# Optimization experiments

Measured on AMD Instinct MI355X. Metric: run time of the kernel, lower is better.

Reference implementation:

```python
import jax, jax.numpy as jnp
import numpy as np

N, E = 50000, 1600000
IN_DIM, HID, L, H = 300, 256, 3, 4
HD = HID // H  # 64
EPS = 1e-5


def setup_inputs() -> dict:
    key = jax.random.key(0)
    ks = jax.random.split(key, 24)
    s = 0.02
    inp = {
        'node_feats': jax.random.normal(ks[0], (N, IN_DIM), jnp.float32),
        'role': jax.random.randint(ks[1], (N,), 0, 3),
        'edge_src': jax.random.randint(ks[2], (E,), 0, N),
        'edge_dst': jax.random.randint(ks[3], (E,), 0, N),
        'edge_weights': jax.random.uniform(ks[4], (E,), jnp.float32),
        # input role transforms (question / entity / context)
        'Wq': jax.random.normal(ks[5], (IN_DIM, HID), jnp.float32) * s,
        'bq': jnp.zeros((HID,), jnp.float32),
        'We': jax.random.normal(ks[6], (IN_DIM, HID), jnp.float32) * s,
        'be': jnp.zeros((HID,), jnp.float32),
        'Wc': jax.random.normal(ks[7], (IN_DIM, HID), jnp.float32) * s,
        'bc': jnp.zeros((HID,), jnp.float32),
        # per-head value projections [H, HID, HD] (q/k projections omitted:
        # softmax over a scalar == 1.0, so they never affect output or grads)
        'Wv': jax.random.normal(ks[8], (H, HID, HD), jnp.float32) * s,
        'bv': jnp.zeros((H, HD), jnp.float32),
        # shared 'default' edge-type transform (the torch code always falls
        # through to 'default' because edata['rel'] entries are tensors)
        'Wd': jax.random.normal(ks[9], (HD, HD), jnp.float32) * s,
        'bd': jnp.zeros((HD,), jnp.float32),
        # attention_output
        'Wo': jax.random.normal(ks[10], (HID, HID), jnp.float32) * s,
        'bo': jnp.zeros((HID,), jnp.float32),
        # GRUCell params (torch layout: [3*HID, in], gate order r,z,n)
        'W_ih': jax.random.normal(ks[11], (3 * HID, HID), jnp.float32) * s,
        'W_hh': jax.random.normal(ks[12], (3 * HID, HID), jnp.float32) * s,
        'b_ih': jnp.zeros((3 * HID,), jnp.float32),
        'b_hh': jnp.zeros((3 * HID,), jnp.float32),
        # per-layer LayerNorm affine params [L, HID]
        'ln_w': jnp.ones((L, HID), jnp.float32),
        'ln_b': jnp.zeros((L, HID), jnp.float32),
    }
    return inp


def _layernorm(x, w, b):
    mu = jnp.mean(x, -1, keepdims=True)
    var = jnp.mean(jnp.square(x - mu), -1, keepdims=True)
    return (x - mu) * jax.lax.rsqrt(var + EPS) * w + b


def _gru_cell(x, hprev, W_ih, W_hh, b_ih, b_hh):
    gi = x @ W_ih.T + b_ih
    gh = hprev @ W_hh.T + b_hh
    i_r, i_z, i_n = jnp.split(gi, 3, axis=-1)
    h_r, h_z, h_n = jnp.split(gh, 3, axis=-1)
    r = jax.nn.sigmoid(i_r + h_r)
    z = jax.nn.sigmoid(i_z + h_z)
    n = jnp.tanh(i_n + r * h_n)
    return (1.0 - z) * n + z * hprev


def reference(node_feats, role, edge_src, edge_dst, edge_weights,
              Wq, bq, We, be, Wc, bc, Wv, bv, Wd, bd, Wo, bo,
              W_ih, W_hh, b_ih, b_hh, ln_w, ln_b):
    n_nodes = node_feats.shape[0]
    # role-dependent input transform: 0=question, 1=evidence/answer, 2=other
    hq = node_feats @ Wq + bq
    he = node_feats @ We + be
    hc = node_feats @ Wc + bc
    r = role[:, None]
    h = jax.nn.relu(jnp.where(r == 0, hq, jnp.where(r == 1, he, hc)))

    path_mem = jax.lax.stop_gradient(h)  # .detach().clone()
    prev_h = h
    num_layers, num_heads = ln_w.shape[0], Wv.shape[0]
    for layer in range(num_layers):
        head_msgs = []
        for hd in range(num_heads):
            # value proj + shared 'default' edge transform (node-level, fused)
            vt = (h @ Wv[hd] + bv[hd]) @ Wd + bd  # [N, HD]
            # scalar softmax == 1.0 -> attn_weight == edge_weight
            msg = vt[edge_src] * edge_weights[:, None]  # [E, HD]
            head_msgs.append(jax.ops.segment_sum(msg, edge_dst,
                                                 num_segments=n_nodes))
        combined = jnp.concatenate(head_msgs, axis=-1)  # [N, HID]
        path_mem = _gru_cell(combined, path_mem, W_ih, W_hh, b_ih, b_hh)
        h = _layernorm(prev_h + combined @ Wo + bo, ln_w[layer], ln_b[layer])
        # dropout: identity in eval mode
        prev_h = h
    return h + path_mem
```

## Files before the change

### kernel.cpp

```cpp
#include <hip/hip_runtime.h>
#include <math.h>

#define NN 50000
#define EE 1600000
#define IND 300
#define KPAD 320
#define NL 3
#define NBLK 785

typedef unsigned short u16;
typedef __attribute__((ext_vector_type(8))) short short8;
typedef __attribute__((ext_vector_type(4))) float floatx4;

__device__ __forceinline__ float b2f(u16 u) {
  union { unsigned i; float f; } v; v.i = ((unsigned)u) << 16; return v.f;
}
__device__ __forceinline__ u16 f2b(float f) {
  union { unsigned i; float f; } v; v.f = f;
  unsigned b = v.i; b += 0x7fffu + ((b >> 16) & 1u);
  return (u16)(b >> 16);
}
__device__ __forceinline__ float sigf(float x) { return 1.0f / (1.0f + __expf(-x)); }

__global__ void count_kernel(const int* __restrict__ dst, int* __restrict__ cnt) {
  int e = blockIdx.x * 256 + threadIdx.x;
  if (e < EE) atomicAdd(&cnt[dst[e]], 1);
}

__global__ __launch_bounds__(256) void scan1_kernel(const int* __restrict__ cnt,
                                                    int* __restrict__ rs,
                                                    int* __restrict__ bsum) {
  __shared__ int ws[4];
  const int t = threadIdx.x, l = t & 63, w = t >> 6;
  const int base = blockIdx.x * 2048 + t * 8;
  int v[8];
  int tot = 0;
  #pragma unroll
  for (int k = 0; k < 8; ++k) {
    int i = base + k;
    v[k] = (i < NN) ? cnt[i] : 0;
    tot += v[k];
  }
  int x = tot;
  #pragma unroll
  for (int off = 1; off < 64; off <<= 1) {
    int y = __shfl_up(x, off);
    if (l >= off) x += y;
  }
  if (l == 63) ws[w] = x;
  __syncthreads();
  int wpre = 0;
  for (int q = 0; q < w; ++q) wpre += ws[q];
  int run = wpre + (x - tot);
  #pragma unroll
  for (int k = 0; k < 8; ++k) {
    int i = base + k;
    if (i < NN) rs[i] = run;
    run += v[k];
  }
  if (t == 255) bsum[blockIdx.x] = wpre + x;
}

__global__ void scan2_kernel(int* __restrict__ bsum, int nb) {
  int l = threadIdx.x;
  int v = (l < nb) ? bsum[l] : 0;
  int x = v;
  #pragma unroll
  for (int off = 1; off < 64; off <<= 1) {
    int y = __shfl_up(x, off);
    if (l >= off) x += y;
  }
  if (l < nb) bsum[l] = x - v;
  if (l == 63) bsum[nb] = x;
}

__global__ void scan3_kernel(const int* __restrict__ bsum, int* __restrict__ rs, int nb) {
  int i = blockIdx.x * 256 + threadIdx.x;
  if (i < NN) rs[i] += bsum[i >> 11];
  if (i == 0) rs[NN] = bsum[nb];
}

__global__ void fill_kernel(const int* __restrict__ dst, const int* __restrict__ rs,
                            int* __restrict__ ncnt, const int* __restrict__ esrc,
                            const float* __restrict__ ew, int2* __restrict__ srcw) {
  int e = blockIdx.x * 256 + threadIdx.x;
  if (e < EE) {
    int d = dst[e];
    int p = atomicAdd(&ncnt[d], 1);
    int2 v;
    v.x = esrc[e];
    v.y = __float_as_int(ew[e]);
    srcw[rs[d] + p] = v;
  }
}

__global__ void role_count(const int* __restrict__ role, int* __restrict__ cnt3) {
  __shared__ int lc[3];
  if (threadIdx.x < 3) lc[threadIdx.x] = 0;
  __syncthreads();
  int i = blockIdx.x * 256 + threadIdx.x;
  if (i < NN) atomicAdd(&lc[role[i]], 1);
  __syncthreads();
  if (threadIdx.x < 3) atomicAdd(&cnt3[threadIdx.x], lc[threadIdx.x]);
}

__global__ void role_plan(const int* __restrict__ cnt3, int* __restrict__ pbase,
                          int* __restrict__ blkrole) {
  __shared__ int pb[4];
  if (threadIdx.x == 0) {
    pb[0] = 0;
    for (int b = 0; b < 3; ++b) pb[b + 1] = pb[b] + (((cnt3[b] + 63) >> 6) << 6);
    for (int b = 0; b < 4; ++b) pbase[b] = pb[b];
  }
  __syncthreads();
  for (int blk = threadIdx.x; blk < NBLK; blk += 256) {
    int m0 = blk * 64;
    int r = -1;
    for (int b = 0; b < 3; ++b)
      if (m0 >= pb[b] && m0 < pb[b + 1]) r = b;
    blkrole[blk] = r;
  }
}

__global__ void role_fill(const int* __restrict__ role, const int* __restrict__ pbase,
                          int* __restrict__ pos3, int* __restrict__ perm) {
  __shared__ int lcnt[3], lbase[3];
  int i = blockIdx.x * 256 + threadIdx.x;
  if (threadIdx.x < 3) lcnt[threadIdx.x] = 0;
  __syncthreads();
  int r = 0, lr = 0;
  bool valid = (i < NN);
  if (valid) {
    r = role[i];
    lr = atomicAdd(&lcnt[r], 1);
  }
  __syncthreads();
  if (threadIdx.x < 3) lbase[threadIdx.x] = atomicAdd(&pos3[threadIdx.x], lcnt[threadIdx.x]);
  __syncthreads();
  if (valid) perm[pbase[r] + lbase[r] + lr] = i;
}

__global__ void xcast_kernel(const float* __restrict__ X, u16* __restrict__ Xb) {
  size_t i = (size_t)blockIdx.x * 256 + threadIdx.x;
  if (i >= (size_t)NN * KPAD) return;
  int r = (int)(i / KPAD), k = (int)(i % KPAD);
  Xb[i] = (k < IND) ? f2b(X[(size_t)r * IND + k]) : (u16)0;
}

__global__ void wt3_kernel(const float* __restrict__ Wq, const float* __restrict__ We,
                           const float* __restrict__ Wc, u16* __restrict__ Wqt,
                           u16* __restrict__ Wet, u16* __restrict__ Wct) {
  int n = blockIdx.x;
  int which = blockIdx.y;
  const float* W = (which == 0) ? Wq : (which == 1) ? We : Wc;
  u16* Wt = (which == 0) ? Wqt : (which == 1) ? Wet : Wct;
  for (int k = threadIdx.x; k < KPAD; k += 256)
    Wt[(size_t)n * KPAD + k] = (k < IND) ? f2b(W[(size_t)k * 256 + n]) : (u16)0;
}

__global__ void wallt_kernel(const float* __restrict__ Wv, const float* __restrict__ Wd,
                             u16* __restrict__ Wallt) {
  int i = blockIdx.x;
  int c = threadIdx.x;
  int hd = c >> 6, j = c & 63;
  const float* wv = &Wv[hd * (256 * 64) + i * 64];
  float s = 0.f;
  #pragma unroll
  for (int m = 0; m < 64; ++m) s = fmaf(wv[m], Wd[m * 64 + j], s);
  Wallt[(size_t)c * 256 + i] = f2b(s);
}

__global__ void ball_kernel(const float* __restrict__ bv, const float* __restrict__ Wd,
                            const float* __restrict__ bd, float* __restrict__ ball) {
  int c = threadIdx.x;
  int hd = c >> 6, j = c & 63;
  float s = bd[j];
  #pragma unroll
  for (int m = 0; m < 64; ++m) s = fmaf(bv[hd * 64 + m], Wd[m * 64 + j], s);
  ball[c] = s;
}

__global__ void wot_kernel(const float* __restrict__ Wo, u16* __restrict__ Wot) {
  int n = blockIdx.x;
  int k = threadIdx.x;
  Wot[(size_t)n * 256 + k] = f2b(Wo[(size_t)k * 256 + n]);
}

__global__ void castbf2_kernel(const float* __restrict__ s0, const float* __restrict__ s1,
                               u16* __restrict__ d0, u16* __restrict__ d1) {
  int i = blockIdx.x * 256 + threadIdx.x;
  const int n = 768 * 256;
  if (i < n) d0[i] = f2b(s0[i]);
  else if (i < 2 * n) d1[i - n] = f2b(s1[i - n]);
}

#define GEMM_PROLOG \
  __shared__ __align__(16) u16 As[64][72]; \
  __shared__ __align__(16) u16 Bs[64][72]; \
  const int t = threadIdx.x; \
  const int lane = t & 63; \
  const int wv_ = t >> 6; \
  const int wr = wv_ >> 1, wc = wv_ & 1; \
  const int l15 = lane & 15, l4 = lane >> 4; \
  const int srow = t >> 2; \
  const int scol = (t & 3) << 4;

#define STAGE_A(AG, ASTRIDE, VALID, ROWIDX, K0) { \
  int4 v0 = {0, 0, 0, 0}, v1 = {0, 0, 0, 0}; \
  if (VALID) { \
    const int4* p_ = (const int4*)&(AG)[(size_t)(ROWIDX) * (ASTRIDE) + (K0) + scol]; \
    v0 = p_[0]; v1 = p_[1]; \
  } \
  *(int4*)&As[srow][scol] = v0; \
  *(int4*)&As[srow][scol + 8] = v1; }

#define STAGE_B(BG, BSTRIDE, ROWIDX, K0) { \
  const int4* p_ = (const int4*)&(BG)[(size_t)(ROWIDX) * (BSTRIDE) + (K0) + scol]; \
  *(int4*)&Bs[srow][scol] = p_[0]; \
  *(int4*)&Bs[srow][scol + 8] = p_[1]; }

#define MFMA_STEP(ACC) { \
  _Pragma("unroll") \
  for (int kc = 0; kc < 2; ++kc) { \
    short8 a0_ = *(const short8*)&As[wr * 32 + 0 + l15][kc * 32 + l4 * 8]; \
    short8 a1_ = *(const short8*)&As[wr * 32 + 16 + l15][kc * 32 + l4 * 8]; \
    short8 b0_ = *(const short8*)&Bs[wc * 32 + 0 + l15][kc * 32 + l4 * 8]; \
    short8 b1_ = *(const short8*)&Bs[wc * 32 + 16 + l15][kc * 32 + l4 * 8]; \
    ACC[0][0] = __builtin_amdgcn_mfma_f32_16x16x32_bf16(a0_, b0_, ACC[0][0], 0, 0, 0); \
    ACC[0][1] = __builtin_amdgcn_mfma_f32_16x16x32_bf16(a0_, b1_, ACC[0][1], 0, 0, 0); \
    ACC[1][0] = __builtin_amdgcn_mfma_f32_16x16x32_bf16(a1_, b0_, ACC[1][0], 0, 0, 0); \
    ACC[1][1] = __builtin_amdgcn_mfma_f32_16x16x32_bf16(a1_, b1_, ACC[1][1], 0, 0, 0); \
  } }

#define GEMM128_PROLOG \
  __shared__ __align__(16) u16 As[128][72]; \
  __shared__ __align__(16) u16 Bs[128][72]; \
  const int t = threadIdx.x; \
  const int lane = t & 63; \
  const int wv_ = t >> 6; \
  const int qr = (wv_ >> 1) * 64, qc = (wv_ & 1) * 64; \
  const int l15 = lane & 15, l4 = lane >> 4; \
  const int srow = t >> 1; \
  const int scol = (t & 1) * 32;

#define STAGE128_A(AG, ASTRIDE, VALID, ROWIDX, K0) { \
  int4 v0 = {0,0,0,0}, v1 = {0,0,0,0}, v2 = {0,0,0,0}, v3 = {0,0,0,0}; \
  if (VALID) { \
    const int4* p_ = (const int4*)&(AG)[(size_t)(ROWIDX) * (ASTRIDE) + (K0) + scol]; \
    v0 = p_[0]; v1 = p_[1]; v2 = p_[2]; v3 = p_[3]; \
  } \
  *(int4*)&As[srow][scol] = v0; *(int4*)&As[srow][scol + 8] = v1; \
  *(int4*)&As[srow][scol + 16] = v2; *(int4*)&As[srow][scol + 24] = v3; }

#define STAGE128_B(BG, BSTRIDE, ROWIDX, K0) { \
  const int4* p_ = (const int4*)&(BG)[(size_t)(ROWIDX) * (BSTRIDE) + (K0) + scol]; \
  *(int4*)&Bs[srow][scol] = p_[0]; *(int4*)&Bs[srow][scol + 8] = p_[1]; \
  *(int4*)&Bs[srow][scol + 16] = p_[2]; *(int4*)&Bs[srow][scol + 24] = p_[3]; }

#define MFMA128_STEP(ACC) { \
  _Pragma("unroll") \
  for (int kc = 0; kc < 2; ++kc) { \
    short8 af_[4], bf_[4]; \
    _Pragma("unroll") \
    for (int m = 0; m < 4; ++m) af_[m] = *(const short8*)&As[qr + m * 16 + l15][kc * 32 + l4 * 8]; \
    _Pragma("unroll") \
    for (int n = 0; n < 4; ++n) bf_[n] = *(const short8*)&Bs[qc + n * 16 + l15][kc * 32 + l4 * 8]; \
    _Pragma("unroll") \
    for (int m = 0; m < 4; ++m) \
      _Pragma("unroll") \
      for (int n = 0; n < 4; ++n) \
        ACC[m][n] = __builtin_amdgcn_mfma_f32_16x16x32_bf16(af_[m], bf_[n], ACC[m][n], 0, 0, 0); \
  } }

__global__ __launch_bounds__(256) void proj_mfma(
    const u16* __restrict__ Xb, const int* __restrict__ perm,
    const int* __restrict__ blkrole,
    const u16* __restrict__ Wqt, const u16* __restrict__ Wet, const u16* __restrict__ Wct,
    const float* __restrict__ bq, const float* __restrict__ be, const float* __restrict__ bc,
    u16* __restrict__ h, u16* __restrict__ pm) {
  const int brole = blkrole[blockIdx.y];
  if (brole < 0) return;
  GEMM_PROLOG
  const int m0 = blockIdx.y * 64;
  const int n0 = blockIdx.x * 64;
  const u16* Bt = (brole == 0) ? Wqt : (brole == 1) ? Wet : Wct;
  const float* bb = (brole == 0) ? bq : (brole == 1) ? be : bc;
  const int prow = perm[m0 + srow];
  floatx4 acc[2][2] = {};
  for (int k0 = 0; k0 < KPAD; k0 += 64) {
    STAGE_A(Xb, KPAD, prow >= 0, prow, k0)
    STAGE_B(Bt, KPAD, n0 + srow, k0)
    __syncthreads();
    MFMA_STEP(acc)
    __syncthreads();
  }
  #pragma unroll
  for (int m = 0; m < 2; ++m)
    #pragma unroll
    for (int reg = 0; reg < 4; ++reg) {
      int gr = m0 + wr * 32 + m * 16 + l4 * 4 + reg;
      int pr = perm[gr];
      if (pr >= 0) {
        #pragma unroll
        for (int n = 0; n < 2; ++n) {
          int c = n0 + wc * 32 + n * 16 + l15;
          float vo = fmaxf(acc[m][n][reg] + bb[c], 0.f);
          u16 ub = f2b(vo);
          h[(size_t)pr * 256 + c] = ub;
          pm[(size_t)pr * 256 + c] = ub;
        }
      }
    }
}

__global__ __launch_bounds__(256) void vgemm_mfma(
    const u16* __restrict__ A, const u16* __restrict__ Bt,
    const float* __restrict__ bias, u16* __restrict__ C) {
  GEMM128_PROLOG
  const int m0 = blockIdx.y * 128;
  const int n0 = blockIdx.x * 128;
  const int ar = m0 + srow;
  floatx4 acc[4][4] = {};
  for (int k0 = 0; k0 < 256; k0 += 64) {
    STAGE128_A(A, 256, ar < NN, ar, k0)
    STAGE128_B(Bt, 256, n0 + srow, k0)
    __syncthreads();
    MFMA128_STEP(acc)
    __syncthreads();
  }
  #pragma unroll
  for (int m = 0; m < 4; ++m)
    #pragma unroll
    for (int reg = 0; reg < 4; ++reg) {
      int gr = m0 + qr + m * 16 + l4 * 4 + reg;
      if (gr < NN) {
        #pragma unroll
        for (int n = 0; n < 4; ++n) {
          int c = n0 + qc + n * 16 + l15;
          C[(size_t)gr * 256 + c] = f2b(acc[m][n][reg] + bias[c]);
        }
      }
    }
}

__global__ __launch_bounds__(256) void agg_kernel(
    const int2* __restrict__ srcw, const int* __restrict__ rs,
    const u16* __restrict__ V, u16* __restrict__ comb) {
  int n = blockIdx.x * 4 + (threadIdx.x >> 6);
  int l = threadIdx.x & 63;
  if (n >= NN) return;
  int s = rs[n], e = rs[n + 1];
  float a0 = 0.f, a1 = 0.f, a2 = 0.f, a3 = 0.f;
  float c0 = 0.f, c1 = 0.f, c2 = 0.f, c3 = 0.f;
  const size_t loff = (size_t)l * 4;
  for (int base = s; base < e; base += 64) {
    int2 p = {0, 0};
    if (base + l < e) p = srcw[base + l];
    int cnt = min(64, e - base);
    int j = 0;
    for (; j + 4 <= cnt; j += 4) {
      int s0 = __shfl(p.x, j + 0), s1 = __shfl(p.x, j + 1);
      int s2 = __shfl(p.x, j + 2), s3 = __shfl(p.x, j + 3);
      float w0 = __int_as_float(__shfl(p.y, j + 0));
      float w1 = __int_as_float(__shfl(p.y, j + 1));
      float w2 = __int_as_float(__shfl(p.y, j + 2));
      float w3 = __int_as_float(__shfl(p.y, j + 3));
      ushort4 v0 = *(const ushort4*)&V[(size_t)s0 * 256 + loff];
      ushort4 v1 = *(const ushort4*)&V[(size_t)s1 * 256 + loff];
      ushort4 v2 = *(const ushort4*)&V[(size_t)s2 * 256 + loff];
      ushort4 v3 = *(const ushort4*)&V[(size_t)s3 * 256 + loff];
      a0 = fmaf(w0, b2f(v0.x), a0); a1 = fmaf(w0, b2f(v0.y), a1);
      a2 = fmaf(w0, b2f(v0.z), a2); a3 = fmaf(w0, b2f(v0.w), a3);
      c0 = fmaf(w1, b2f(v1.x), c0); c1 = fmaf(w1, b2f(v1.y), c1);
      c2 = fmaf(w1, b2f(v1.z), c2); c3 = fmaf(w1, b2f(v1.w), c3);
      a0 = fmaf(w2, b2f(v2.x), a0); a1 = fmaf(w2, b2f(v2.y), a1);
      a2 = fmaf(w2, b2f(v2.z), a2); a3 = fmaf(w2, b2f(v2.w), a3);
      c0 = fmaf(w3, b2f(v3.x), c0); c1 = fmaf(w3, b2f(v3.y), c1);
      c2 = fmaf(w3, b2f(v3.z), c2); c3 = fmaf(w3, b2f(v3.w), c3);
    }
    for (; j < cnt; ++j) {
      int src = __shfl(p.x, j);
      float w = __int_as_float(__shfl(p.y, j));
      ushort4 v = *(const ushort4*)&V[(size_t)src * 256 + loff];
      a0 = fmaf(w, b2f(v.x), a0); a1 = fmaf(w, b2f(v.y), a1);
      a2 = fmaf(w, b2f(v.z), a2); a3 = fmaf(w, b2f(v.w), a3);
    }
  }
  a0 += c0; a1 += c1; a2 += c2; a3 += c3;
  ushort4 o;
  o.x = f2b(a0); o.y = f2b(a1); o.z = f2b(a2); o.w = f2b(a3);
  *(ushort4*)&comb[(size_t)n * 256 + loff] = o;
}

__global__ __launch_bounds__(256) void grurz_mfma(
    const u16* __restrict__ comb, const u16* __restrict__ pmc,
    const u16* __restrict__ Wiht, const u16* __restrict__ Whht,
    const float* __restrict__ bih, const float* __restrict__ bhh,
    u16* __restrict__ R, u16* __restrict__ Z) {
  GEMM128_PROLOG
  const int m0 = blockIdx.y * 128;
  const int j0 = blockIdx.x * 128;
  const int ar = m0 + srow;
  floatx4 acc[4][4] = {};
  #pragma unroll
  for (int p = 0; p < 2; ++p) {
    const u16* Ag = p ? pmc : comb;
    const u16* Bt = p ? Whht : Wiht;
    for (int k0 = 0; k0 < 256; k0 += 64) {
      STAGE128_A(Ag, 256, ar < NN, ar, k0)
      STAGE128_B(Bt, 256, j0 + srow, k0)
      __syncthreads();
      MFMA128_STEP(acc)
      __syncthreads();
    }
  }
  #pragma unroll
  for (int m = 0; m < 4; ++m)
    #pragma unroll
    for (int reg = 0; reg < 4; ++reg) {
      int gr = m0 + qr + m * 16 + l4 * 4 + reg;
      if (gr < NN) {
        #pragma unroll
        for (int n = 0; n < 4; ++n) {
          int j = j0 + qc + n * 16 + l15;
          float g = sigf(acc[m][n][reg] + bih[j] + bhh[j]);
          if (j < 256) R[(size_t)gr * 256 + j] = f2b(g);
          else         Z[(size_t)gr * 256 + (j - 256)] = f2b(g);
        }
      }
    }
}

__global__ __launch_bounds__(256) void grun_mfma(
    const u16* __restrict__ comb, const u16* __restrict__ pmc,
    const u16* __restrict__ Wiht, const u16* __restrict__ Whht,
    const float* __restrict__ bih, const float* __restrict__ bhh,
    const u16* __restrict__ R, const u16* __restrict__ Z,
    u16* __restrict__ pmn) {
  GEMM128_PROLOG
  const int m0 = blockIdx.y * 128;
  const int n0 = blockIdx.x * 128;
  const int ar = m0 + srow;
  floatx4 ai[4][4] = {};
  floatx4 ah[4][4] = {};
  for (int k0 = 0; k0 < 256; k0 += 64) {
    STAGE128_A(comb, 256, ar < NN, ar, k0)
    STAGE128_B(Wiht, 256, 512 + n0 + srow, k0)
    __syncthreads();
    MFMA128_STEP(ai)
    __syncthreads();
  }
  for (int k0 = 0; k0 < 256; k0 += 64) {
    STAGE128_A(pmc, 256, ar < NN, ar, k0)
    STAGE128_B(Whht, 256, 512 + n0 + srow, k0)
    __syncthreads();
    MFMA128_STEP(ah)
    __syncthreads();
  }
  #pragma unroll
  for (int m = 0; m < 4; ++m)
    #pragma unroll
    for (int reg = 0; reg < 4; ++reg) {
      int gr = m0 + qr + m * 16 + l4 * 4 + reg;
      if (gr < NN) {
        #pragma unroll
        for (int n = 0; n < 4; ++n) {
          int c = n0 + qc + n * 16 + l15;
          float i_n = ai[m][n][reg] + bih[512 + c];
          float h_n = ah[m][n][reg] + bhh[512 + c];
          float rg = b2f(R[(size_t)gr * 256 + c]);
          float z = b2f(Z[(size_t)gr * 256 + c]);
          float po = b2f(pmc[(size_t)gr * 256 + c]);
          float nn2 = tanhf(i_n + rg * h_n);
          pmn[(size_t)gr * 256 + c] = f2b((1.f - z) * nn2 + z * po);
        }
      }
    }
}

__global__ __launch_bounds__(256) void wo_mfma(
    const u16* __restrict__ comb, const u16* __restrict__ Wot,
    const float* __restrict__ bo, const u16* __restrict__ h,
    u16* __restrict__ tmp) {
  GEMM128_PROLOG
  const int m0 = blockIdx.y * 128;
  const int n0 = blockIdx.x * 128;
  const int ar = m0 + srow;
  floatx4 acc[4][4] = {};
  for (int k0 = 0; k0 < 256; k0 += 64) {
    STAGE128_A(comb, 256, ar < NN, ar, k0)
    STAGE128_B(Wot, 256, n0 + srow, k0)
    __syncthreads();
    MFMA128_STEP(acc)
    __syncthreads();
  }
  #pragma unroll
  for (int m = 0; m < 4; ++m)
    #pragma unroll
    for (int reg = 0; reg < 4; ++reg) {
      int gr = m0 + qr + m * 16 + l4 * 4 + reg;
      if (gr < NN) {
        #pragma unroll
        for (int n = 0; n < 4; ++n) {
          int c = n0 + qc + n * 16 + l15;
          float v = acc[m][n][reg] + bo[c] + b2f(h[(size_t)gr * 256 + c]);
          tmp[(size_t)gr * 256 + c] = f2b(v);
        }
      }
    }
}

__global__ __launch_bounds__(256) void ln_kernel(
    const u16* __restrict__ tmp, u16* __restrict__ h,
    const float* __restrict__ lnw, const float* __restrict__ lnb) {
  int n = blockIdx.x * 4 + (threadIdx.x >> 6);
  int l = threadIdx.x & 63;
  if (n >= NN) return;
  ushort4 v = *(const ushort4*)&tmp[(size_t)n * 256 + l * 4];
  float x0 = b2f(v.x), x1 = b2f(v.y), x2 = b2f(v.z), x3 = b2f(v.w);
  float s = x0 + x1 + x2 + x3;
  #pragma unroll
  for (int off = 1; off < 64; off <<= 1) s += __shfl_xor(s, off);
  float mu = s * (1.f / 256.f);
  float d0 = x0 - mu, d1 = x1 - mu, d2 = x2 - mu, d3 = x3 - mu;
  float vs = d0 * d0 + d1 * d1 + d2 * d2 + d3 * d3;
  #pragma unroll
  for (int off = 1; off < 64; off <<= 1) vs += __shfl_xor(vs, off);
  float inv = rsqrtf(vs * (1.f / 256.f) + 1e-5f);
  int c = l * 4;
  ushort4 o;
  o.x = f2b(d0 * inv * lnw[c + 0] + lnb[c + 0]);
  o.y = f2b(d1 * inv * lnw[c + 1] + lnb[c + 1]);
  o.z = f2b(d2 * inv * lnw[c + 2] + lnb[c + 2]);
  o.w = f2b(d3 * inv * lnw[c + 3] + lnb[c + 3]);
  *(ushort4*)&h[(size_t)n * 256 + c] = o;
}

__global__ __launch_bounds__(256) void ln_final_kernel(
    const u16* __restrict__ tmp, const u16* __restrict__ pm,
    const float* __restrict__ lnw, const float* __restrict__ lnb,
    float* __restrict__ out) {
  int n = blockIdx.x * 4 + (threadIdx.x >> 6);
  int l = threadIdx.x & 63;
  if (n >= NN) return;
  ushort4 v = *(const ushort4*)&tmp[(size_t)n * 256 + l * 4];
  float x0 = b2f(v.x), x1 = b2f(v.y), x2 = b2f(v.z), x3 = b2f(v.w);
  float s = x0 + x1 + x2 + x3;
  #pragma unroll
  for (int off = 1; off < 64; off <<= 1) s += __shfl_xor(s, off);
  float mu = s * (1.f / 256.f);
  float d0 = x0 - mu, d1 = x1 - mu, d2 = x2 - mu, d3 = x3 - mu;
  float vs = d0 * d0 + d1 * d1 + d2 * d2 + d3 * d3;
  #pragma unroll
  for (int off = 1; off < 64; off <<= 1) vs += __shfl_xor(vs, off);
  float inv = rsqrtf(vs * (1.f / 256.f) + 1e-5f);
  int c = l * 4;
  ushort4 pv = *(const ushort4*)&pm[(size_t)n * 256 + c];
  float4 o;
  o.x = b2f(f2b(d0 * inv * lnw[c + 0] + lnb[c + 0])) + b2f(pv.x);
  o.y = b2f(f2b(d1 * inv * lnw[c + 1] + lnb[c + 1])) + b2f(pv.y);
  o.z = b2f(f2b(d2 * inv * lnw[c + 2] + lnb[c + 2])) + b2f(pv.z);
  o.w = b2f(f2b(d3 * inv * lnw[c + 3] + lnb[c + 3])) + b2f(pv.w);
  *(float4*)&out[(size_t)n * 256 + c] = o;
}

extern "C" void kernel_launch(void* const* d_in, const int* in_sizes, int n_in,
                              void* d_out, int out_size, void* d_ws, size_t ws_size,
                              hipStream_t stream) {
  const float* node_feats = (const float*)d_in[0];
  const int* role = (const int*)d_in[1];
  const int* esrc = (const int*)d_in[2];
  const int* edst = (const int*)d_in[3];
  const float* ew = (const float*)d_in[4];
  const float* Wq = (const float*)d_in[5];
  const float* bq = (const float*)d_in[6];
  const float* We = (const float*)d_in[7];
  const float* be = (const float*)d_in[8];
  const float* Wc = (const float*)d_in[9];
  const float* bc = (const float*)d_in[10];
  const float* Wv = (const float*)d_in[11];
  const float* bv = (const float*)d_in[12];
  const float* Wd = (const float*)d_in[13];
  const float* bd = (const float*)d_in[14];
  const float* Wo = (const float*)d_in[15];
  const float* bo = (const float*)d_in[16];
  const float* Wih = (const float*)d_in[17];
  const float* Whh = (const float*)d_in[18];
  const float* bih = (const float*)d_in[19];
  const float* bhh = (const float*)d_in[20];
  const float* lnw = (const float*)d_in[21];
  const float* lnb = (const float*)d_in[22];
  float* out = (float*)d_out;

  char* ws = (char*)d_ws;
  size_t off = 0;
  auto take = [&](size_t bytes) {
    char* p = ws + off;
    off = (off + bytes + 511) & ~(size_t)511;
    return p;
  };
  const size_t NC2 = (size_t)NN * 256 * 2;
  u16* Xb = (u16*)take((size_t)NN * KPAD * 2);
  u16* h = (u16*)take(NC2);
  u16* pm0 = (u16*)take(NC2);
  u16* pm1 = (u16*)take(NC2);
  u16* V = (u16*)take(NC2);
  u16* comb = (u16*)take(NC2);
  u16* Z = (u16*)take(NC2);
  u16* tmp = (u16*)take(NC2);
  u16* Wqt = (u16*)take((size_t)256 * KPAD * 2);
  u16* Wet = (u16*)take((size_t)256 * KPAD * 2);
  u16* Wct = (u16*)take((size_t)256 * KPAD * 2);
  u16* Wallt = (u16*)take((size_t)256 * 256 * 2);
  u16* Wot = (u16*)take((size_t)256 * 256 * 2);
  u16* Wiht = (u16*)take((size_t)768 * 256 * 2);
  u16* Whht = (u16*)take((size_t)768 * 256 * 2);
  float* ball = (float*)take(256 * 4);
  int* cnt = (int*)take((size_t)NN * 4);
  int* rs = (int*)take((size_t)(NN + 1) * 4);
  int* ncnt = (int*)take((size_t)NN * 4);
  int2* srcw = (int2*)take((size_t)EE * 8);
  int* cnt3 = (int*)take(16);
  int* pos3 = (int*)take(16);
  int* pbase = (int*)take(16);
  int* blkrole = (int*)take((size_t)NBLK * 4);
  int* perm = (int*)take((size_t)NBLK * 64 * 4);
  int* bsum = (int*)take(64 * 4);
  u16* R = V;

  const int NB_SCAN = (NN + 2047) / 2048;

  hipMemsetAsync(cnt, 0, (size_t)NN * 4, stream);
  hipMemsetAsync(ncnt, 0, (size_t)NN * 4, stream);
  hipMemsetAsync(cnt3, 0, 16, stream);
  hipMemsetAsync(pos3, 0, 16, stream);
  hipMemsetAsync(perm, 0xFF, (size_t)NBLK * 64 * 4, stream);

  count_kernel<<<(EE + 255) / 256, 256, 0, stream>>>(edst, cnt);
  scan1_kernel<<<NB_SCAN, 256, 0, stream>>>(cnt, rs, bsum);
  scan2_kernel<<<1, 64, 0, stream>>>(bsum, NB_SCAN);
  scan3_kernel<<<(NN + 255) / 256, 256, 0, stream>>>(bsum, rs, NB_SCAN);
  fill_kernel<<<(EE + 255) / 256, 256, 0, stream>>>(edst, rs, ncnt, esrc, ew, srcw);

  role_count<<<(NN + 255) / 256, 256, 0, stream>>>(role, cnt3);
  role_plan<<<1, 256, 0, stream>>>(cnt3, pbase, blkrole);
  role_fill<<<(NN + 255) / 256, 256, 0, stream>>>(role, pbase, pos3, perm);

  xcast_kernel<<<(int)(((size_t)NN * KPAD + 255) / 256), 256, 0, stream>>>(node_feats, Xb);
  wt3_kernel<<<dim3(256, 3), 256, 0, stream>>>(Wq, We, Wc, Wqt, Wet, Wct);
  wallt_kernel<<<256, 256, 0, stream>>>(Wv, Wd, Wallt);
  ball_kernel<<<1, 256, 0, stream>>>(bv, Wd, bd, ball);
  wot_kernel<<<256, 256, 0, stream>>>(Wo, Wot);
  castbf2_kernel<<<(2 * 768 * 256 + 255) / 256, 256, 0, stream>>>(Wih, Whh, Wiht, Whht);

  proj_mfma<<<dim3(4, NBLK), 256, 0, stream>>>(Xb, perm, blkrole, Wqt, Wet, Wct,
                                               bq, be, bc, h, pm0);

  u16* pmc = pm0;
  u16* pmn = pm1;
  const int MB128 = (NN + 127) / 128;
  for (int layer = 0; layer < NL; ++layer) {
    vgemm_mfma<<<dim3(2, MB128), 256, 0, stream>>>(h, Wallt, ball, V);
    agg_kernel<<<(NN + 3) / 4, 256, 0, stream>>>(srcw, rs, V, comb);
    grurz_mfma<<<dim3(4, MB128), 256, 0, stream>>>(comb, pmc, Wiht, Whht, bih, bhh, R, Z);
    grun_mfma<<<dim3(2, MB128), 256, 0, stream>>>(comb, pmc, Wiht, Whht, bih, bhh, R, Z, pmn);
    wo_mfma<<<dim3(2, MB128), 256, 0, stream>>>(comb, Wot, bo, h, tmp);
    if (layer < NL - 1) {
      ln_kernel<<<(NN + 3) / 4, 256, 0, stream>>>(tmp, h, lnw + layer * 256, lnb + layer * 256);
    } else {
      ln_final_kernel<<<(NN + 3) / 4, 256, 0, stream>>>(tmp, pmn, lnw + layer * 256,
                                                        lnb + layer * 256, out);
    }
    u16* sw = pmc; pmc = pmn; pmn = sw;
  }
}
```

Baseline: 1.190 ms.

## Fuse GRU gate kernels into one MFMA kernel and split aggregation by column half

Merges the two GRU kernels (r/z gates, then n gate) into a single MFMA kernel. Each block computes all six gate tiles for 64 rows by 64 columns, so the R and Z intermediate bf16 buffers are never written to or read back from global memory. It also splits the edge aggregation into two column-half launches. Each wave now loads 2 bf16 values per edge instead of 4, which doubles the number of blocks and the edge-index re-reads but gives finer gathers. The fused GEMM uses smaller 64-row tiles with larger LDS use and more accumulators, which may reduce occupancy.

```diff
diff --git a/kernel.cpp b/kernel.cpp
--- a/kernel.cpp
+++ b/kernel.cpp
@@ -7,6 +7,7 @@
 #define KPAD 320
 #define NL 3
 #define NBLK 785
+#define AGG_NB 12500
 
 typedef unsigned short u16;
 typedef __attribute__((ext_vector_type(8))) short short8;
@@ -346,13 +347,15 @@
 __global__ __launch_bounds__(256) void agg_kernel(
     const int2* __restrict__ srcw, const int* __restrict__ rs,
     const u16* __restrict__ V, u16* __restrict__ comb) {
-  int n = blockIdx.x * 4 + (threadIdx.x >> 6);
+  int bid = blockIdx.x;
+  int slice = (bid >= AGG_NB) ? 1 : 0;
+  int nb = bid - slice * AGG_NB;
+  int n = nb * 4 + (threadIdx.x >> 6);
   int l = threadIdx.x & 63;
   if (n >= NN) return;
   int s = rs[n], e = rs[n + 1];
-  float a0 = 0.f, a1 = 0.f, a2 = 0.f, a3 = 0.f;
-  float c0 = 0.f, c1 = 0.f, c2 = 0.f, c3 = 0.f;
-  const size_t loff = (size_t)l * 4;
+  const size_t coff = (size_t)(slice << 7) + l * 2;
+  float a0 = 0.f, a1 = 0.f, c0 = 0.f, c1 = 0.f;
   for (int base = s; base < e; base += 64) {
     int2 p = {0, 0};
     if (base + l < e) p = srcw[base + l];
@@ -365,113 +368,114 @@
       float w1 = __int_as_float(__shfl(p.y, j + 1));
       float w2 = __int_as_float(__shfl(p.y, j + 2));
       float w3 = __int_as_float(__shfl(p.y, j + 3));
-      ushort4 v0 = *(const ushort4*)&V[(size_t)s0 * 256 + loff];
-      ushort4 v1 = *(const ushort4*)&V[(size_t)s1 * 256 + loff];
-      ushort4 v2 = *(const ushort4*)&V[(size_t)s2 * 256 + loff];
-      ushort4 v3 = *(const ushort4*)&V[(size_t)s3 * 256 + loff];
+      ushort2 v0 = *(const ushort2*)&V[(size_t)s0 * 256 + coff];
+      ushort2 v1 = *(const ushort2*)&V[(size_t)s1 * 256 + coff];
+      ushort2 v2 = *(const ushort2*)&V[(size_t)s2 * 256 + coff];
+      ushort2 v3 = *(const ushort2*)&V[(size_t)s3 * 256 + coff];
       a0 = fmaf(w0, b2f(v0.x), a0); a1 = fmaf(w0, b2f(v0.y), a1);
-      a2 = fmaf(w0, b2f(v0.z), a2); a3 = fmaf(w0, b2f(v0.w), a3);
       c0 = fmaf(w1, b2f(v1.x), c0); c1 = fmaf(w1, b2f(v1.y), c1);
-      c2 = fmaf(w1, b2f(v1.z), c2); c3 = fmaf(w1, b2f(v1.w), c3);
       a0 = fmaf(w2, b2f(v2.x), a0); a1 = fmaf(w2, b2f(v2.y), a1);
-      a2 = fmaf(w2, b2f(v2.z), a2); a3 = fmaf(w2, b2f(v2.w), a3);
       c0 = fmaf(w3, b2f(v3.x), c0); c1 = fmaf(w3, b2f(v3.y), c1);
-      c2 = fmaf(w3, b2f(v3.z), c2); c3 = fmaf(w3, b2f(v3.w), c3);
     }
     for (; j < cnt; ++j) {
       int src = __shfl(p.x, j);
       float w = __int_as_float(__shfl(p.y, j));
-      ushort4 v = *(const ushort4*)&V[(size_t)src * 256 + loff];
+      ushort2 v = *(const ushort2*)&V[(size_t)src * 256 + coff];
       a0 = fmaf(w, b2f(v.x), a0); a1 = fmaf(w, b2f(v.y), a1);
-      a2 = fmaf(w, b2f(v.z), a2); a3 = fmaf(w, b2f(v.w), a3);
-    }
-  }
-  a0 += c0; a1 += c1; a2 += c2; a3 += c3;
-  ushort4 o;
-  o.x = f2b(a0); o.y = f2b(a1); o.z = f2b(a2); o.w = f2b(a3);
-  *(ushort4*)&comb[(size_t)n * 256 + loff] = o;
-}
-
-__global__ __launch_bounds__(256) void grurz_mfma(
+    }
+  }
+  a0 += c0; a1 += c1;
+  ushort2 o;
+  o.x = f2b(a0); o.y = f2b(a1);
+  *(ushort2*)&comb[(size_t)n * 256 + coff] = o;
+}
+
+__global__ __launch_bounds__(256) void gru_mfma(
     const u16* __restrict__ comb, const u16* __restrict__ pmc,
     const u16* __restrict__ Wiht, const u16* __restrict__ Whht,
     const float* __restrict__ bih, const float* __restrict__ bhh,
-    u16* __restrict__ R, u16* __restrict__ Z) {
-  GEMM128_PROLOG
-  const int m0 = blockIdx.y * 128;
-  const int j0 = blockIdx.x * 128;
+    u16* __restrict__ pmn) {
+  __shared__ __align__(16) u16 As[2][64][72];
+  __shared__ __align__(16) u16 Bs[6][64][72];
+  const int t = threadIdx.x;
+  const int lane = t & 63;
+  const int wv_ = t >> 6;
+  const int wr = wv_ >> 1, wc = wv_ & 1;
+  const int l15 = lane & 15, l4 = lane >> 4;
+  const int srow = t >> 2;
+  const int scol = (t & 3) << 4;
+  const int m0 = blockIdx.y * 64;
+  const int cb = blockIdx.x;
   const int ar = m0 + srow;
-  floatx4 acc[4][4] = {};
-  #pragma unroll
-  for (int p = 0; p < 2; ++p) {
-    const u16* Ag = p ? pmc : comb;
-    const u16* Bt = p ? Whht : Wiht;
-    for (int k0 = 0; k0 < 256; k0 += 64) {
-      STAGE128_A(Ag, 256, ar < NN, ar, k0)
-      STAGE128_B(Bt, 256, j0 + srow, k0)
-      __syncthreads();
-      MFMA128_STEP(acc)
-      __syncthreads();
-    }
-  }
-  #pragma unroll
-  for (int m = 0; m < 4; ++m)
+  const bool av = ar < NN;
+  floatx4 acc[6][2][2] = {};
+  for (int k0 = 0; k0 < 256; k0 += 64) {
+    {
+      int4 v0 = {0,0,0,0}, v1 = {0,0,0,0}, u0 = {0,0,0,0}, u1 = {0,0,0,0};
+      if (av) {
+        const int4* pa = (const int4*)&comb[(size_t)ar * 256 + k0 + scol];
+        v0 = pa[0]; v1 = pa[1];
+        const int4* pb = (const int4*)&pmc[(size_t)ar * 256 + k0 + scol];
+        u0 = pb[0]; u1 = pb[1];
+      }
+      *(int4*)&As[0][srow][scol] = v0; *(int4*)&As[0][srow][scol + 8] = v1;
+      *(int4*)&As[1][srow][scol] = u0; *(int4*)&As[1][srow][scol + 8] = u1;
+    }
+    #pragma unroll
+    for (int g = 0; g < 3; ++g) {
+      size_t row = (size_t)(g * 256 + cb * 64 + srow);
+      const int4* p1 = (const int4*)&Wiht[row * 256 + k0 + scol];
+      *(int4*)&Bs[g][srow][scol] = p1[0];
+      *(int4*)&Bs[g][srow][scol + 8] = p1[1];
+      const int4* p2 = (const int4*)&Whht[row * 256 + k0 + scol];
+      *(int4*)&Bs[3 + g][srow][scol] = p2[0];
+      *(int4*)&Bs[3 + g][srow][scol + 8] = p2[1];
+    }
+    __syncthreads();
+    #pragma unroll
+    for (int kc = 0; kc < 2; ++kc) {
+      short8 a0f[2], a1f[2];
+      #pragma unroll
+      for (int m = 0; m < 2; ++m) {
+        a0f[m] = *(const short8*)&As[0][wr * 32 + m * 16 + l15][kc * 32 + l4 * 8];
+        a1f[m] = *(const short8*)&As[1][wr * 32 + m * 16 + l15][kc * 32 + l4 * 8];
+      }
+      #pragma unroll
+      for (int g = 0; g < 3; ++g) {
+        short8 b0 = *(const short8*)&Bs[g][wc * 32 + 0 + l15][kc * 32 + l4 * 8];
+        short8 b1 = *(const short8*)&Bs[g][wc * 32 + 16 + l15][kc * 32 + l4 * 8];
+        acc[g][0][0] = __builtin_amdgcn_mfma_f32_16x16x32_bf16(a0f[0], b0, acc[g][0][0], 0, 0, 0);
+        acc[g][0][1] = __builtin_amdgcn_mfma_f32_16x16x32_bf16(a0f[0], b1, acc[g][0][1], 0, 0, 0);
+        acc[g][1][0] = __builtin_amdgcn_mfma_f32_16x16x32_bf16(a0f[1], b0, acc[g][1][0], 0, 0, 0);
+        acc[g][1][1] = __builtin_amdgcn_mfma_f32_16x16x32_bf16(a0f[1], b1, acc[g][1][1], 0, 0, 0);
+      }
+      #pragma unroll
+      for (int g = 3; g < 6; ++g) {
+        short8 b0 = *(const short8*)&Bs[g][wc * 32 + 0 + l15][kc * 32 + l4 * 8];
+        short8 b1 = *(const short8*)&Bs[g][wc * 32 + 16 + l15][kc * 32 + l4 * 8];
+        acc[g][0][0] = __builtin_amdgcn_mfma_f32_16x16x32_bf16(a1f[0], b0, acc[g][0][0], 0, 0, 0);
+        acc[g][0][1] = __builtin_amdgcn_mfma_f32_16x16x32_bf16(a1f[0], b1, acc[g][0][1], 0, 0, 0);
+        acc[g][1][0] = __builtin_amdgcn_mfma_f32_16x16x32_bf16(a1f[1], b0, acc[g][1][0], 0, 0, 0);
+        acc[g][1][1] = __builtin_amdgcn_mfma_f32_16x16x32_bf16(a1f[1], b1, acc[g][1][1], 0, 0, 0);
+      }
+    }
+    __syncthreads();
+  }
+  #pragma unroll
+  for (int m = 0; m < 2; ++m)
     #pragma unroll
     for (int reg = 0; reg < 4; ++reg) {
-      int gr = m0 + qr + m * 16 + l4 * 4 + reg;
+      int gr = m0 + wr * 32 + m * 16 + l4 * 4 + reg;
       if (gr < NN) {
         #pragma unroll
-        for (int n = 0; n < 4; ++n) {
-          int j = j0 + qc + n * 16 + l15;
-          float g = sigf(acc[m][n][reg] + bih[j] + bhh[j]);
-          if (j < 256) R[(size_t)gr * 256 + j] = f2b(g);
-          else         Z[(size_t)gr * 256 + (j - 256)] = f2b(g);
-        }
-      }
-    }
-}
-
-__global__ __launch_bounds__(256) void grun_mfma(
-    const u16* __restrict__ comb, const u16* __restrict__ pmc,
-    const u16* __restrict__ Wiht, const u16* __restrict__ Whht,
-    const float* __restrict__ bih, const float* __restrict__ bhh,
-    const u16* __restrict__ R, const u16* __restrict__ Z,
-    u16* __restrict__ pmn) {
-  GEMM128_PROLOG
-  const int m0 = blockIdx.y * 128;
-  const int n0 = blockIdx.x * 128;
-  const int ar = m0 + srow;
-  floatx4 ai[4][4] = {};
-  floatx4 ah[4][4] = {};
-  for (int k0 = 0; k0 < 256; k0 += 64) {
-    STAGE128_A(comb, 256, ar < NN, ar, k0)
-    STAGE128_B(Wiht, 256, 512 + n0 + srow, k0)
-    __syncthreads();
-    MFMA128_STEP(ai)
-    __syncthreads();
-  }
-  for (int k0 = 0; k0 < 256; k0 += 64) {
-    STAGE128_A(pmc, 256, ar < NN, ar, k0)
-    STAGE128_B(Whht, 256, 512 + n0 + srow, k0)
-    __syncthreads();
-    MFMA128_STEP(ah)
-    __syncthreads();
-  }
-  #pragma unroll
-  for (int m = 0; m < 4; ++m)
-    #pragma unroll
-    for (int reg = 0; reg < 4; ++reg) {
-      int gr = m0 + qr + m * 16 + l4 * 4 + reg;
-      if (gr < NN) {
-        #pragma unroll
-        for (int n = 0; n < 4; ++n) {
-          int c = n0 + qc + n * 16 + l15;
-          float i_n = ai[m][n][reg] + bih[512 + c];
-          float h_n = ah[m][n][reg] + bhh[512 + c];
-          float rg = b2f(R[(size_t)gr * 256 + c]);
-          float z = b2f(Z[(size_t)gr * 256 + c]);
+        for (int n = 0; n < 2; ++n) {
+          int c = cb * 64 + wc * 32 + n * 16 + l15;
+          float r = sigf(acc[0][m][n][reg] + acc[3][m][n][reg] + bih[c] + bhh[c]);
+          float z = sigf(acc[1][m][n][reg] + acc[4][m][n][reg] + bih[256 + c] + bhh[256 + c]);
+          float i_n = acc[2][m][n][reg] + bih[512 + c];
+          float h_n = acc[5][m][n][reg] + bhh[512 + c];
+          float nn2 = tanhf(i_n + r * h_n);
           float po = b2f(pmc[(size_t)gr * 256 + c]);
-          float nn2 = tanhf(i_n + rg * h_n);
           pmn[(size_t)gr * 256 + c] = f2b((1.f - z) * nn2 + z * po);
         }
       }
@@ -606,7 +610,6 @@
   u16* pm1 = (u16*)take(NC2);
   u16* V = (u16*)take(NC2);
   u16* comb = (u16*)take(NC2);
-  u16* Z = (u16*)take(NC2);
   u16* tmp = (u16*)take(NC2);
   u16* Wqt = (u16*)take((size_t)256 * KPAD * 2);
   u16* Wet = (u16*)take((size_t)256 * KPAD * 2);
@@ -626,7 +629,6 @@
   int* blkrole = (int*)take((size_t)NBLK * 4);
   int* perm = (int*)take((size_t)NBLK * 64 * 4);
   int* bsum = (int*)take(64 * 4);
-  u16* R = V;
 
   const int NB_SCAN = (NN + 2047) / 2048;
 
@@ -659,11 +661,11 @@
   u16* pmc = pm0;
   u16* pmn = pm1;
   const int MB128 = (NN + 127) / 128;
+  const int MB64 = (NN + 63) / 64;
   for (int layer = 0; layer < NL; ++layer) {
     vgemm_mfma<<<dim3(2, MB128), 256, 0, stream>>>(h, Wallt, ball, V);
-    agg_kernel<<<(NN + 3) / 4, 256, 0, stream>>>(srcw, rs, V, comb);
-    grurz_mfma<<<dim3(4, MB128), 256, 0, stream>>>(comb, pmc, Wiht, Whht, bih, bhh, R, Z);
-    grun_mfma<<<dim3(2, MB128), 256, 0, stream>>>(comb, pmc, Wiht, Whht, bih, bhh, R, Z, pmn);
+    agg_kernel<<<2 * AGG_NB, 256, 0, stream>>>(srcw, rs, V, comb);
+    gru_mfma<<<dim3(4, MB64), 256, 0, stream>>>(comb, pmc, Wiht, Whht, bih, bhh, pmn);
     wo_mfma<<<dim3(2, MB128), 256, 0, stream>>>(comb, Wot, bo, h, tmp);
     if (layer < NL - 1) {
       ln_kernel<<<(NN + 3) / 4, 256, 0, stream>>>(tmp, h, lnw + layer * 256, lnb + layer * 256);
```

New measurement: 1.032 ms. -13.3%, faster.
